# Kernel optimization log

Hardware: AMD Instinct MI355X
Metric: run time of the kernel (lower is better)

Reference implementation:

```python
import jax, jax.numpy as jnp
import numpy as np

BS, S = 8, 1024
D_MODEL, N_HEADS, D_K = 256, 8, 32
H_SHARED, H_SEL = 2, 2
N_DYN = N_HEADS - H_SHARED
D_FF = 1024
N_BLOCKS = 2
L = 3 * N_BLOCKS  # blocks_1 (N_BLOCKS layers) + blocks_2 (2*N_BLOCKS layers)
NEG = -1e9


def _layernorm(x, g, b):
    m = x.mean(-1, keepdims=True)
    v = ((x - m) ** 2).mean(-1, keepdims=True)
    return (x - m) * jax.lax.rsqrt(v + 1e-5) * g + b


def _layer(p, mask_val, query, values, q4router, apply_pos):
    (Wq, bq, Wv, bv, Wg, Wo, bo, g1, be1, Wf1, bf1, Wf2, bf2, g2, be2) = p
    bs, s, dm = query.shape
    q = query @ Wq + bq            # kq_same=True -> k = q
    v = values @ Wv + bv
    qh = q.reshape(bs, s, N_HEADS, D_K).transpose(0, 2, 1, 3)   # [b,h,s,d]
    vh = v.reshape(bs, s, N_HEADS, D_K).transpose(0, 2, 1, 3)
    scores = jnp.einsum('bhqd,bhkd->bhqk', qh, qh) / (D_K ** 0.5)
    # nopeek = triu(ones,k=mask); allowed where nopeek==0 -> col < row + mask
    allowed = jnp.arange(s)[None, :] < (jnp.arange(s)[:, None] + mask_val)
    scores = jnp.where(allowed[None, None], scores, NEG)
    attnw = jax.nn.softmax(scores, axis=-1)
    # head routing: replicate torch view->permute->reshape order exactly
    qr = q4router.reshape(bs, s, N_HEADS, D_K).transpose(0, 2, 1, 3).reshape(bs * s, N_HEADS * D_K)
    gates = jax.nn.softmax(qr @ Wg, axis=1)                     # [bs*s, N_DYN]
    _, idx = jax.lax.top_k(gates, H_SEL)
    dyn_mask = jax.nn.one_hot(idx, N_DYN, dtype=gates.dtype).sum(axis=1)
    dyn_scores = gates * dyn_mask
    hs = dyn_mask.sum(axis=0)
    hp = gates.mean(axis=0)
    bal = ((hs / (hs.sum() + 1e-5)) * (hp / (hp.sum() + 1e-5))).sum()
    routing = jnp.concatenate(
        [jnp.ones((bs, s, H_SHARED), gates.dtype), dyn_scores.reshape(bs, s, N_DYN)], axis=-1)
    routing = routing.mean(axis=1)[:, :, None, None]            # [b,h,1,1]
    out = jnp.einsum('bhqk,bhkd->bhqd', attnw, vh) * routing
    out = out.transpose(0, 2, 1, 3).reshape(bs, s, dm) @ Wo + bo
    query = _layernorm(query + out, g1, be1)
    if apply_pos:
        ff = jax.nn.relu(query @ Wf1 + bf1) @ Wf2 + bf2
        query = _layernorm(query + ff, g2, be2)
    return query, bal


def _forward(q_embed_data, qa_embed_data, Wq, bq, Wv, bv, Wg, Wo, bo,
             ln1_w, ln1_b, Wf1, bf1, Wf2, bf2, ln2_w, ln2_b):
    stacks = (Wq, bq, Wv, bv, Wg, Wo, bo, ln1_w, ln1_b, Wf1, bf1, Wf2, bf2, ln2_w, ln2_b)
    params = [tuple(a[i] for a in stacks) for i in range(L)]
    x, y = q_embed_data, qa_embed_data
    for i in range(N_BLOCKS):
        y, _ = _layer(params[i], 1, y, y, x, True)
    attn = jnp.zeros((), jnp.float32)
    li = N_BLOCKS
    for _ in range(N_BLOCKS):
        x, _ = _layer(params[li], 1, x, x, x, False)  # self-block, no FFN
        li += 1
        x, attn = _layer(params[li], 0, x, y, x, True)  # cross to y, strict causal
        li += 1
    return x, attn


def setup_inputs():
    key = jax.random.key(0)
    ks = jax.random.split(key, 10)
    w = lambda k, shp: (jax.random.normal(k, shp, jnp.float32) * 0.02)
    return {
        'q_embed_data': jax.random.normal(ks[0], (BS, S, D_MODEL), jnp.float32),
        'qa_embed_data': jax.random.normal(ks[1], (BS, S, D_MODEL), jnp.float32),
        'Wq': w(ks[2], (L, D_MODEL, D_MODEL)), 'bq': jnp.zeros((L, D_MODEL), jnp.float32),
        'Wv': w(ks[3], (L, D_MODEL, D_MODEL)), 'bv': jnp.zeros((L, D_MODEL), jnp.float32),
        'Wg': w(ks[4], (L, D_MODEL, N_DYN)),
        'Wo': w(ks[5], (L, D_MODEL, D_MODEL)), 'bo': jnp.zeros((L, D_MODEL), jnp.float32),
        'ln1_w': jnp.ones((L, D_MODEL), jnp.float32), 'ln1_b': jnp.zeros((L, D_MODEL), jnp.float32),
        'Wf1': w(ks[6], (L, D_MODEL, D_FF)), 'bf1': jnp.zeros((L, D_FF), jnp.float32),
        'Wf2': w(ks[7], (L, D_FF, D_MODEL)), 'bf2': jnp.zeros((L, D_MODEL), jnp.float32),
        'ln2_w': jnp.ones((L, D_MODEL), jnp.float32), 'ln2_b': jnp.zeros((L, D_MODEL), jnp.float32),
    }


def reference(q_embed_data, qa_embed_data, Wq, bq, Wv, bv, Wg, Wo, bo,
              ln1_w, ln1_b, Wf1, bf1, Wf2, bf2, ln2_w, ln2_b):
    return _forward(q_embed_data, qa_embed_data, Wq, bq, Wv, bv, Wg, Wo, bo,
                    ln1_w, ln1_b, Wf1, bf1, Wf2, bf2, ln2_w, ln2_b)
```

## Files before the change

kernel.cpp:

```cpp
#include <hip/hip_runtime.h>


constexpr int DMODEL = 256;
constexpr int SEQ    = 1024;
constexpr int BATCH  = 8;
constexpr int NHEADS = 8;
constexpr int DKDIM  = 32;
constexpr int NDYN_C = 6;
constexpr int NTOK_C = BATCH * SEQ;
constexpr int DFF_C  = 1024;

using frag_bf16 = __attribute__((ext_vector_type(8))) short;
using f32x4    = __attribute__((ext_vector_type(4))) float;
typedef unsigned short ushort_t;

__device__ __forceinline__ ushort_t f2bf(float f) {
  unsigned u = __float_as_uint(f);
  unsigned r = (u + 0x7fffu + ((u >> 16) & 1u)) >> 16;
  return (ushort_t)r;
}

__device__ __forceinline__ unsigned cvt_pk_bf16(float lo, float hi) {
  unsigned r;
  asm("v_cvt_pk_bf16_f32 %0, %1, %2" : "=v"(r) : "v"(lo), "v"(hi));
  return r;
}

#define GLOAD_LDS16(gsrc, ldst)                                             \
  __builtin_amdgcn_global_load_lds(                                         \
      (const __attribute__((address_space(1))) void*)(gsrc),                \
      (__attribute__((address_space(3))) void*)(ldst), 16, 0, 0)

#define SYNC_DRAIN()                                                        \
  do {                                                                      \
    asm volatile("s_waitcnt vmcnt(0) lgkmcnt(0)" ::: "memory");             \
    __builtin_amdgcn_sched_barrier(0);                                      \
    __syncthreads();                                                        \
  } while (0)

__device__ __forceinline__
void gemm_body(int mode, int bx, int by,
               const ushort_t* __restrict__ A, const ushort_t* __restrict__ B,
               const float* __restrict__ bias, void* __restrict__ Cp,
               int M, int N, int K,
               ushort_t (*sA)[4096], ushort_t (*sB)[4096]) {
  const int tid = threadIdx.x;
  const int wid = tid >> 6, lane = tid & 63;
  const int li = lane & 15, g = lane >> 4;
  const int wr = wid >> 1, wc = wid & 1;
  const int m0 = by * 64, n0 = bx * 64;
  f32x4 acc[2][2] = {};
  const int srow = wid * 8 + (lane >> 3);
  const int schk = (lane & 7) ^ (lane >> 3);
  const ushort_t* gA1 = &A[(size_t)(m0 + srow) * K + schk * 8];
  const ushort_t* gA2 = &A[(size_t)(m0 + 32 + srow) * K + schk * 8];
  const ushort_t* gB1 = &B[(size_t)(n0 + srow) * K + schk * 8];
  const ushort_t* gB2 = &B[(size_t)(n0 + 32 + srow) * K + schk * 8];
  const int nk = K >> 6;

  GLOAD_LDS16(gA1, sA[0] + wid * 512);
  GLOAD_LDS16(gA2, sA[0] + 2048 + wid * 512);
  GLOAD_LDS16(gB1, sB[0] + wid * 512);
  GLOAD_LDS16(gB2, sB[0] + 2048 + wid * 512);
  SYNC_DRAIN();

  auto compute = [&](int cur) {
#pragma unroll
    for (int s = 0; s < 2; ++s) {
      frag_bf16 af[2], bf[2];
#pragma unroll
      for (int m = 0; m < 2; ++m) {
        const int row = wr * 32 + m * 16 + li;
        af[m] = *reinterpret_cast<const frag_bf16*>(
            &sA[cur][row * 64 + ((s * 4 + g) ^ (row & 7)) * 8]);
      }
#pragma unroll
      for (int n = 0; n < 2; ++n) {
        const int row = wc * 32 + n * 16 + li;
        bf[n] = *reinterpret_cast<const frag_bf16*>(
            &sB[cur][row * 64 + ((s * 4 + g) ^ (row & 7)) * 8]);
      }
#pragma unroll
      for (int m = 0; m < 2; ++m)
#pragma unroll
        for (int n = 0; n < 2; ++n)
          acc[m][n] = __builtin_amdgcn_mfma_f32_16x16x32_bf16(af[m], bf[n], acc[m][n], 0, 0, 0);
    }
  };

  for (int kt = 0; kt < nk - 1; ++kt) {
    const int cur = kt & 1;
    const int k1 = (kt + 1) << 6;
    GLOAD_LDS16(gA1 + k1, sA[cur ^ 1] + wid * 512);
    GLOAD_LDS16(gA2 + k1, sA[cur ^ 1] + 2048 + wid * 512);
    GLOAD_LDS16(gB1 + k1, sB[cur ^ 1] + wid * 512);
    GLOAD_LDS16(gB2 + k1, sB[cur ^ 1] + 2048 + wid * 512);
    compute(cur);
    SYNC_DRAIN();
  }
  compute((nk - 1) & 1);

  constexpr float QSCALE = 0.42044820762685725f;
#pragma unroll
  for (int m = 0; m < 2; ++m)
#pragma unroll
    for (int n = 0; n < 2; ++n)
#pragma unroll
      for (int r = 0; r < 4; ++r) {
        const int mg = m0 + wr * 32 + m * 16 + g * 4 + r;
        const int ng = n0 + wc * 32 + n * 16 + li;
        if (mode == 0) {
          ((float*)Cp)[(size_t)mg * N + ng] = acc[m][n][r] + bias[ng];
        } else if (mode == 1) {
          ((ushort_t*)Cp)[(size_t)mg * N + ng] = f2bf((acc[m][n][r] + bias[ng]) * QSCALE);
        } else if (mode == 2) {
          ((ushort_t*)Cp)[(size_t)mg * N + ng] = f2bf(fmaxf(acc[m][n][r] + bias[ng], 0.0f));
        } else {
          ((ushort_t*)Cp)[((size_t)((ng >> 10) * 256 + mg)) * SEQ + (ng & 1023)] =
              f2bf(acc[m][n][r] + bias[mg]);
        }
      }
}

__global__ __launch_bounds__(256)
void gemm_mfma_k(int mode, const ushort_t* __restrict__ A, const ushort_t* __restrict__ B,
                 const float* __restrict__ bias, void* __restrict__ Cp,
                 int M, int N, int K) {
  __shared__ ushort_t sA[2][4096];
  __shared__ ushort_t sB[2][4096];
  gemm_body(mode, blockIdx.x, blockIdx.y, A, B, bias, Cp, M, N, K, sA, sB);
}

__device__ __forceinline__
void router_body(const float* __restrict__ R, const float* __restrict__ Wg,
                 float* __restrict__ partials, float* sW, float (*red)[128]) {
  const int tid = threadIdx.x;
  for (int t = tid; t < DMODEL * NDYN_C; t += 256) sW[t] = Wg[t];
  __syncthreads();
  if (tid < 128) {
    const int r = blockIdx.x * 128 + tid;
    const int b = r >> 10;
    const int h = (r >> 7) & 7;
    const int s8 = r & 127;
    float lg[NDYN_C] = {};
    for (int t8 = 0; t8 < 8; ++t8) {
      const float* base = &R[((size_t)(b * SEQ + s8 * 8 + t8)) * DMODEL + h * DKDIM];
#pragma unroll
      for (int d = 0; d < DKDIM; ++d) {
        const float x = base[d];
        const float* w = &sW[(t8 * 32 + d) * NDYN_C];
#pragma unroll
        for (int j = 0; j < NDYN_C; ++j) lg[j] = fmaf(x, w[j], lg[j]);
      }
    }
    float mx = lg[0];
#pragma unroll
    for (int j = 1; j < NDYN_C; ++j) mx = fmaxf(mx, lg[j]);
    float e[NDYN_C], sum = 0.0f;
#pragma unroll
    for (int j = 0; j < NDYN_C; ++j) { e[j] = expf(lg[j] - mx); sum += e[j]; }
    float g[NDYN_C];
#pragma unroll
    for (int j = 0; j < NDYN_C; ++j) g[j] = e[j] / sum;
    int j1 = 0;
#pragma unroll
    for (int j = 1; j < NDYN_C; ++j) if (g[j] > g[j1]) j1 = j;
    int j2 = -1;
#pragma unroll
    for (int j = 0; j < NDYN_C; ++j) {
      if (j == j1) continue;
      if (j2 < 0 || g[j] > g[j2]) j2 = j;
    }
#pragma unroll
    for (int j = 0; j < NDYN_C; ++j) {
      const bool sel = (j == j1) || (j == j2);
      red[j][tid] = sel ? g[j] : 0.0f;
      red[6 + j][tid] = sel ? 1.0f : 0.0f;
      red[12 + j][tid] = g[j];
    }
  }
  __syncthreads();
  if (tid < 18) {
    float s = 0.0f;
    for (int i = 0; i < 128; ++i) s += red[tid][i];
    partials[blockIdx.x * 18 + tid] = s;
  }
}

__global__ __launch_bounds__(256)
void gemm_qv_router_k(const ushort_t* __restrict__ Aq, const ushort_t* __restrict__ Bq,
                      const float* __restrict__ biasq, void* __restrict__ Cq,
                      const ushort_t* __restrict__ Av, const ushort_t* __restrict__ Bv,
                      const float* __restrict__ biasv, void* __restrict__ Cv,
                      const float* __restrict__ R, const float* __restrict__ Wg,
                      float* __restrict__ partials) {
  __shared__ ushort_t sA[2][4096];
  __shared__ ushort_t sB[2][4096];
  if (blockIdx.y == 4) {
    if (blockIdx.z == 0 && blockIdx.x < 64) {
      float* sW = (float*)&sA[0][0];
      float (*red)[128] = (float(*)[128])&sB[0][0];
      router_body(R, Wg, partials, sW, red);
    }
    return;
  }
  if (blockIdx.z == 0)
    gemm_body(1, blockIdx.y, blockIdx.x, Aq, Bq, biasq, Cq, NTOK_C, DMODEL, DMODEL, sA, sB);
  else
    gemm_body(3, blockIdx.x, blockIdx.y, Av, Bv, biasv, Cv, DMODEL, NTOK_C, DMODEL, sA, sB);
}

__device__ __forceinline__
void transpose_body(const float* __restrict__ ip, ushort_t* __restrict__ op, int R, int C,
                    int c0, int r0) {
  __shared__ float t[32][33];
  const int tx = threadIdx.x & 31, ty = threadIdx.x >> 5;
#pragma unroll
  for (int i = 0; i < 4; ++i) t[ty + 8 * i][tx] = ip[(size_t)(r0 + ty + 8 * i) * C + c0 + tx];
  __syncthreads();
#pragma unroll
  for (int i = 0; i < 4; ++i)
    op[(size_t)(c0 + ty + 8 * i) * R + r0 + tx] = f2bf(t[tx][ty + 8 * i]);
}

__global__ __launch_bounds__(256)
void transpose_k(const float* __restrict__ in, ushort_t* __restrict__ out, int R, int C) {
  const int z = blockIdx.z;
  transpose_body(in + (size_t)z * R * C, out + (size_t)z * R * C, R, C,
                 blockIdx.x * 32, blockIdx.y * 32);
}

__global__ __launch_bounds__(256)
void transpose3_k(const float* __restrict__ W0, ushort_t* __restrict__ O0,
                  const float* __restrict__ W1, ushort_t* __restrict__ O1,
                  const float* __restrict__ W2, ushort_t* __restrict__ O2) {
  const int z = blockIdx.z;
  const int zi = z / 6, zz = z % 6;
  const float* in = (zi == 0) ? W0 : (zi == 1) ? W1 : W2;
  ushort_t* out = (zi == 0) ? O0 : (zi == 1) ? O1 : O2;
  transpose_body(in + (size_t)zz * DMODEL * DMODEL, out + (size_t)zz * DMODEL * DMODEL,
                 DMODEL, DMODEL, blockIdx.x * 32, blockIdx.y * 32);
}

__global__ __launch_bounds__(256)
void conv_init_k(const float* __restrict__ s0, float* __restrict__ f0,
                 ushort_t* __restrict__ b0,
                 const float* __restrict__ s1, float* __restrict__ f1,
                 ushort_t* __restrict__ b1) {
  const float* src = blockIdx.y ? s1 : s0;
  float* dstF = blockIdx.y ? f1 : f0;
  ushort_t* dstB = blockIdx.y ? b1 : b0;
  const int i = blockIdx.x * 256 + threadIdx.x;
  const float4 v = reinterpret_cast<const float4*>(src)[i];
  reinterpret_cast<float4*>(dstF)[i] = v;
  ushort4 b;
  b.x = f2bf(v.x); b.y = f2bf(v.y); b.z = f2bf(v.z); b.w = f2bf(v.w);
  reinterpret_cast<ushort4*>(dstB)[i] = b;
}

__global__ __launch_bounds__(256)
void attn_mfma_k(const ushort_t* __restrict__ qb, const ushort_t* __restrict__ vbT,
                 const float* __restrict__ partials, ushort_t* __restrict__ out,
                 int mask_val) {
  __shared__ ushort_t sk[2][2048];
  __shared__ ushort_t sv[2][2048];
  __shared__ ushort_t pbuf[4096];
  const int gid = blockIdx.x;
  const int b = gid & 7;
  const int slot = gid >> 3;
  const int h = (slot >> 4) & 7;
  const int qblk = 15 - (slot & 15);
  const int q0 = qblk * 64;
  const int tid = threadIdx.x;
  const int wave = tid >> 6, lane = tid & 63;
  const int g = lane >> 4, li = lane & 15;
  const int qw = q0 + wave * 16;
  const int qrow = qw + li;

  const frag_bf16 qf = *reinterpret_cast<const frag_bf16*>(
      &qb[((size_t)(b * SEQ + qrow)) * DMODEL + h * DKDIM + g * 8]);

  float mrun = -INFINITY, lrun = 0.f;
  f32x4 o0 = {0.f, 0.f, 0.f, 0.f}, o1 = {0.f, 0.f, 0.f, 0.f};
  ushort_t* pP = &pbuf[wave * 1024];

  const ushort_t* gK = &qb[((size_t)(b * SEQ + wave * 16 + li)) * DMODEL + h * DKDIM + g * 8];
  const ushort_t* gV = &vbT[((size_t)((b * NHEADS + h) * DKDIM) + wave * 8 + (lane >> 3)) * SEQ
                            + ((lane & 7) ^ (lane >> 3)) * 8];

  const int nt = qblk + 1;
  GLOAD_LDS16(gK, sk[0] + wave * 512);
  GLOAD_LDS16(gV, sv[0] + wave * 512);
  SYNC_DRAIN();

  auto tile_step = [&](int t, int cur) {
    const int kt = t * 64;
    f32x4 s[4];
#pragma unroll
    for (int kb = 0; kb < 4; ++kb) {
      frag_bf16 kf = *reinterpret_cast<const frag_bf16*>(&sk[cur][(kb * 64 + g * 16 + li) * 8]);
      f32x4 z = {0.f, 0.f, 0.f, 0.f};
      s[kb] = __builtin_amdgcn_mfma_f32_16x16x32_bf16(kf, qf, z, 0, 0, 0);
    }
    const bool need_mask = (kt + 63) >= (qw + mask_val);
    if (need_mask) {
#pragma unroll
      for (int kb = 0; kb < 4; ++kb)
#pragma unroll
        for (int r = 0; r < 4; ++r) {
          const int col = kt + kb * 16 + 4 * g + r;
          if (col >= (qrow + mask_val)) s[kb][r] = -1e9f;
        }
    }
    float tm = -INFINITY;
#pragma unroll
    for (int kb = 0; kb < 4; ++kb)
#pragma unroll
      for (int r = 0; r < 4; ++r) tm = fmaxf(tm, s[kb][r]);
    tm = fmaxf(tm, __shfl_xor(tm, 16, 64));
    tm = fmaxf(tm, __shfl_xor(tm, 32, 64));
    const float mnew = fmaxf(mrun, tm);
    const float scl = __expf(mrun - mnew);
    float p[4][4];
    float psum = 0.f;
#pragma unroll
    for (int kb = 0; kb < 4; ++kb)
#pragma unroll
      for (int r = 0; r < 4; ++r) { p[kb][r] = __expf(s[kb][r] - mnew); psum += p[kb][r]; }
    psum += __shfl_xor(psum, 16, 64);
    psum += __shfl_xor(psum, 32, 64);
    lrun = lrun * scl + psum;
    mrun = mnew;
#pragma unroll
    for (int r = 0; r < 4; ++r) { o0[r] *= scl; o1[r] *= scl; }
#pragma unroll
    for (int kb = 0; kb < 4; ++kb)
#pragma unroll
      for (int pair = 0; pair < 2; ++pair) {
        const unsigned pk = cvt_pk_bf16(p[kb][2 * pair], p[kb][2 * pair + 1]);
        const int addr = (((kb >> 1) * 4 + (kb & 1) * 2 + (g >> 1)) * 16 + li) * 8
                         + 4 * (g & 1) + 2 * pair;
        *reinterpret_cast<unsigned*>(&pP[addr]) = pk;
      }
    __threadfence_block();
#pragma unroll
    for (int c = 0; c < 2; ++c) {
      frag_bf16 pf = *reinterpret_cast<const frag_bf16*>(&pP[((c * 4 + g) * 16 + li) * 8]);
      frag_bf16 vf0 = *reinterpret_cast<const frag_bf16*>(
          &sv[cur][li * 64 + ((4 * c + g) ^ (li & 7)) * 8]);
      frag_bf16 vf1 = *reinterpret_cast<const frag_bf16*>(
          &sv[cur][(16 + li) * 64 + ((4 * c + g) ^ (li & 7)) * 8]);
      o0 = __builtin_amdgcn_mfma_f32_16x16x32_bf16(vf0, pf, o0, 0, 0, 0);
      o1 = __builtin_amdgcn_mfma_f32_16x16x32_bf16(vf1, pf, o1, 0, 0, 0);
    }
  };

  for (int t = 0; t < nt - 1; ++t) {
    const int cur = t & 1;
    const int kt = t * 64;
    GLOAD_LDS16(gK + (size_t)(kt + 64) * DMODEL, sk[cur ^ 1] + wave * 512);
    GLOAD_LDS16(gV + (kt + 64), sv[cur ^ 1] + wave * 512);
    tile_step(t, cur);
    SYNC_DRAIN();
  }
  tile_step(nt - 1, (nt - 1) & 1);

  float rt = 1.0f;
  if (h >= 2) {
    const int j = h - 2;
    float sr = 0.f;
#pragma unroll
    for (int t = 0; t < 8; ++t) sr += partials[(b * 8 + t) * 18 + j];
    rt = sr * (1.0f / 1024.0f);
  }
  const float mult = rt / lrun;
  if (!(mask_val == 0 && qrow == 0)) {
    const size_t base = (size_t)(b * SEQ + qrow) * DMODEL + h * DKDIM;
    ushort4 w0, w1;
    w0.x = f2bf(o0[0] * mult); w0.y = f2bf(o0[1] * mult);
    w0.z = f2bf(o0[2] * mult); w0.w = f2bf(o0[3] * mult);
    w1.x = f2bf(o1[0] * mult); w1.y = f2bf(o1[1] * mult);
    w1.z = f2bf(o1[2] * mult); w1.w = f2bf(o1[3] * mult);
    *reinterpret_cast<ushort4*>(&out[base + 4 * g]) = w0;
    *reinterpret_cast<ushort4*>(&out[base + 16 + 4 * g]) = w1;
  }
  if (mask_val == 0 && qblk == 0 && wave == 0) {
    const int d = lane >> 1, hf = lane & 1;
    const ushort_t* src = &vbT[(((size_t)(b * NHEADS + h)) * DKDIM + d) * SEQ + hf * 512];
    float s = 0.f;
    for (int k = 0; k < 512; k += 8) {
      frag_bf16 v = *reinterpret_cast<const frag_bf16*>(&src[k]);
#pragma unroll
      for (int j = 0; j < 8; ++j)
        s += __uint_as_float(((unsigned)(ushort_t)v[j]) << 16);
    }
    s += __shfl_xor(s, 1, 64);
    if (hf == 0)
      out[(size_t)(b * SEQ) * DMODEL + h * DKDIM + d] = f2bf(s * (1.0f / 1024.0f) * rt);
  }
}

__global__ void router_reduce_k(const float* __restrict__ partials,
                                float* __restrict__ bal_out) {
  const int tid = threadIdx.x;
  if (tid == 0) {
    float hs[6], hp[6];
    float hssum = 0.0f, hpsum = 0.0f;
    for (int j = 0; j < 6; ++j) {
      float a = 0.0f, c = 0.0f;
      for (int bi = 0; bi < 64; ++bi) {
        a += partials[bi * 18 + 6 + j];
        c += partials[bi * 18 + 12 + j];
      }
      hs[j] = a;
      hp[j] = c * (1.0f / 8192.0f);
      hssum += hs[j];
      hpsum += hp[j];
    }
    float bal = 0.0f;
    for (int j = 0; j < 6; ++j)
      bal += (hs[j] / (hssum + 1e-5f)) * (hp[j] / (hpsum + 1e-5f));
    *bal_out = bal;
  }
}

__global__ __launch_bounds__(256)
void add_ln_k(const float* __restrict__ Xin, float* __restrict__ Xout,
              ushort_t* __restrict__ Xbf, const float* __restrict__ Y,
              const float* __restrict__ g, const float* __restrict__ be) {
  const int wave = threadIdx.x >> 6, lane = threadIdx.x & 63;
  const int r = blockIdx.x * 4 + wave;
  const size_t base = (size_t)r * DMODEL + lane * 4;
  float4 x = *reinterpret_cast<const float4*>(&Xin[base]);
  const float4 y = *reinterpret_cast<const float4*>(&Y[base]);
  x.x += y.x; x.y += y.y; x.z += y.z; x.w += y.w;
  float s = x.x + x.y + x.z + x.w;
#pragma unroll
  for (int o = 32; o >= 1; o >>= 1) s += __shfl_xor(s, o, 64);
  const float mean = s * (1.0f / DMODEL);
  const float4 d = {x.x - mean, x.y - mean, x.z - mean, x.w - mean};
  float v = d.x * d.x + d.y * d.y + d.z * d.z + d.w * d.w;
#pragma unroll
  for (int o = 32; o >= 1; o >>= 1) v += __shfl_xor(v, o, 64);
  const float rstd = 1.0f / sqrtf(v * (1.0f / DMODEL) + 1e-5f);
  const float4 gg = *reinterpret_cast<const float4*>(&g[lane * 4]);
  const float4 bb = *reinterpret_cast<const float4*>(&be[lane * 4]);
  float4 rv;
  rv.x = d.x * rstd * gg.x + bb.x;
  rv.y = d.y * rstd * gg.y + bb.y;
  rv.z = d.z * rstd * gg.z + bb.z;
  rv.w = d.w * rstd * gg.w + bb.w;
  *reinterpret_cast<float4*>(&Xout[base]) = rv;
  ushort4 o4;
  o4.x = f2bf(rv.x); o4.y = f2bf(rv.y); o4.z = f2bf(rv.z); o4.w = f2bf(rv.w);
  *reinterpret_cast<ushort4*>(&Xbf[base]) = o4;
}

extern "C" void kernel_launch(void* const* d_in, const int* in_sizes, int n_in,
                              void* d_out, int out_size, void* d_ws, size_t ws_size,
                              hipStream_t stream) {
  const float* q_embed  = (const float*)d_in[0];
  const float* qa_embed = (const float*)d_in[1];
  const float* Wq  = (const float*)d_in[2];
  const float* bq  = (const float*)d_in[3];
  const float* Wv  = (const float*)d_in[4];
  const float* bv  = (const float*)d_in[5];
  const float* Wg  = (const float*)d_in[6];
  const float* Wo  = (const float*)d_in[7];
  const float* bo  = (const float*)d_in[8];
  const float* ln1w = (const float*)d_in[9];
  const float* ln1b = (const float*)d_in[10];
  const float* Wf1 = (const float*)d_in[11];
  const float* bf1 = (const float*)d_in[12];
  const float* Wf2 = (const float*)d_in[13];
  const float* bf2 = (const float*)d_in[14];
  const float* ln2w = (const float*)d_in[15];
  const float* ln2b = (const float*)d_in[16];
  float* out = (float*)d_out;

  const size_t NA = (size_t)NTOK_C * DMODEL;
  float* xbuf = (float*)d_ws;
  float* ybuf = xbuf + NA;
  float* ob   = ybuf + NA;
  float* routing8   = ob + NA;
  float* partials   = routing8 + 64;
  float* balscratch = partials + 64 * 18;
  ushort_t* xbf   = (ushort_t*)(balscratch + 16);
  ushort_t* ybf   = xbf + NA;
  ushort_t* qb_bf = ybf + NA;
  ushort_t* vbT   = qb_bf + NA;
  ushort_t* ab_bf = vbT + NA;
  ushort_t* hb    = ab_bf + NA;
  ushort_t* WqT   = hb + (size_t)NTOK_C * DFF_C;
  ushort_t* WvT   = WqT + (size_t)6 * DMODEL * DMODEL;
  ushort_t* WoT   = WvT + (size_t)6 * DMODEL * DMODEL;
  ushort_t* Wf1T  = WoT + (size_t)6 * DMODEL * DMODEL;
  ushort_t* Wf2T  = Wf1T + (size_t)6 * DMODEL * DFF_C;

  transpose3_k<<<dim3(8, 8, 18), 256, 0, stream>>>(Wq, WqT, Wv, WvT, Wo, WoT);
  transpose_k<<<dim3(32, 8, 6), 256, 0, stream>>>(Wf1, Wf1T, DMODEL, DFF_C);
  transpose_k<<<dim3(8, 32, 6), 256, 0, stream>>>(Wf2, Wf2T, DFF_C, DMODEL);
  conv_init_k<<<dim3(NA / 1024, 2), 256, 0, stream>>>(q_embed, xbuf, xbf,
                                                      qa_embed, ybuf, ybf);

  auto run_layer = [&](int l, float* Q, ushort_t* Qbf, const ushort_t* Vbf,
                       int mask_val, bool ffn, bool last) {
    const float* bq_l = bq + (size_t)l * DMODEL;
    const float* bv_l = bv + (size_t)l * DMODEL;
    const float* Wg_l = Wg + (size_t)l * DMODEL * NDYN_C;
    const float* bo_l = bo + (size_t)l * DMODEL;
    const float* g1_l = ln1w + (size_t)l * DMODEL;
    const float* b1_l = ln1b + (size_t)l * DMODEL;
    const ushort_t* WqT_l = WqT + (size_t)l * DMODEL * DMODEL;
    const ushort_t* WvT_l = WvT + (size_t)l * DMODEL * DMODEL;
    const ushort_t* WoT_l = WoT + (size_t)l * DMODEL * DMODEL;

    gemm_qv_router_k<<<dim3(128, 5, 2), 256, 0, stream>>>(
        Qbf, WqT_l, bq_l, qb_bf, WvT_l, Vbf, bv_l, vbT, xbuf, Wg_l, partials);
    if (last)
      router_reduce_k<<<1, 64, 0, stream>>>(partials, out + NA);
    attn_mfma_k<<<1024, 256, 0, stream>>>(qb_bf, vbT, partials, ab_bf, mask_val);
    gemm_mfma_k<<<dim3(4, 128), 256, 0, stream>>>(
        0, ab_bf, WoT_l, bo_l, ob, NTOK_C, DMODEL, DMODEL);
    add_ln_k<<<NTOK_C / 4, 256, 0, stream>>>(Q, Q, Qbf, ob, g1_l, b1_l);
    if (ffn) {
      const float* bf1_l = bf1 + (size_t)l * DFF_C;
      const float* bf2_l = bf2 + (size_t)l * DMODEL;
      const float* g2_l = ln2w + (size_t)l * DMODEL;
      const float* b2_l = ln2b + (size_t)l * DMODEL;
      const ushort_t* Wf1T_l = Wf1T + (size_t)l * DMODEL * DFF_C;
      const ushort_t* Wf2T_l = Wf2T + (size_t)l * DFF_C * DMODEL;
      gemm_mfma_k<<<dim3(16, 128), 256, 0, stream>>>(
          2, Qbf, Wf1T_l, bf1_l, hb, NTOK_C, DFF_C, DMODEL);
      gemm_mfma_k<<<dim3(4, 128), 256, 0, stream>>>(
          0, hb, Wf2T_l, bf2_l, ob, NTOK_C, DMODEL, DFF_C);
      add_ln_k<<<NTOK_C / 4, 256, 0, stream>>>(Q, last ? out : Q, Qbf, ob, g2_l, b2_l);
    }
  };

  run_layer(0, ybuf, ybf, ybf, 1, true, false);
  run_layer(1, ybuf, ybf, ybf, 1, true, false);
  run_layer(2, xbuf, xbf, xbf, 1, false, false);
  run_layer(3, xbuf, xbf, ybf, 0, true, false);
  run_layer(4, xbuf, xbf, xbf, 1, false, false);
  run_layer(5, xbuf, xbf, ybf, 0, true, true);
}
```

Measured before the change: 547.1 us.

## Fuse output/FFN2 GEMMs with residual add and LayerNorm epilogue

Adds a GEMM kernel where each block computes a full 32-row by 256-column output tile, so the residual add and LayerNorm can run in the epilogue using cross-wave shared-memory reductions. It replaces the separate Wo and Wf2 GEMMs plus add_ln kernels, which removes the float intermediate round-trip through global memory and one launch per use. In exchange the grid drops to 256 blocks with a large B tile in LDS, which lowers parallelism and occupancy. Variance is now computed as E[x^2]-mean^2, which is less numerically stable.

```diff
diff --git a/kernel.cpp b/kernel.cpp
--- a/kernel.cpp
+++ b/kernel.cpp
@@ -131,6 +131,125 @@
   gemm_body(mode, blockIdx.x, blockIdx.y, A, B, bias, Cp, M, N, K, sA, sB);
 }
 
+__global__ __launch_bounds__(256)
+void gemm_ln_k(const ushort_t* __restrict__ A, const ushort_t* __restrict__ B,
+               const float* __restrict__ bias,
+               const float* __restrict__ Xin, float* __restrict__ Xout,
+               ushort_t* __restrict__ Xbf,
+               const float* __restrict__ gam, const float* __restrict__ bet,
+               int K) {
+  __shared__ ushort_t sA[2][2048];
+  __shared__ ushort_t sB[2][16384];
+  __shared__ float ws1[4][32];
+  __shared__ float ws2[4][32];
+  const int tid = threadIdx.x;
+  const int wid = tid >> 6, lane = tid & 63;
+  const int li = lane & 15, g = lane >> 4;
+  const int wc = wid;
+  const int m0 = blockIdx.x * 32;
+  f32x4 acc[2][4] = {};
+  const int srow = tid >> 3;
+  const int schk = (tid & 7) ^ (srow & 7);
+  const ushort_t* gA = &A[(size_t)(m0 + srow) * K + schk * 8];
+  const ushort_t* gB = &B[(size_t)srow * K + schk * 8];
+  const int nk = K >> 6;
+
+  GLOAD_LDS16(gA, sA[0] + wid * 512);
+#pragma unroll
+  for (int i = 0; i < 8; ++i)
+    GLOAD_LDS16(gB + (size_t)i * 32 * K, sB[0] + i * 2048 + wid * 512);
+  SYNC_DRAIN();
+
+  auto compute = [&](int cur) {
+#pragma unroll
+    for (int s = 0; s < 2; ++s) {
+      frag_bf16 af[2], bf[4];
+#pragma unroll
+      for (int m = 0; m < 2; ++m) {
+        const int row = m * 16 + li;
+        af[m] = *reinterpret_cast<const frag_bf16*>(
+            &sA[cur][row * 64 + ((s * 4 + g) ^ (row & 7)) * 8]);
+      }
+#pragma unroll
+      for (int n = 0; n < 4; ++n) {
+        const int row = wc * 64 + n * 16 + li;
+        bf[n] = *reinterpret_cast<const frag_bf16*>(
+            &sB[cur][row * 64 + ((s * 4 + g) ^ (row & 7)) * 8]);
+      }
+#pragma unroll
+      for (int m = 0; m < 2; ++m)
+#pragma unroll
+        for (int n = 0; n < 4; ++n)
+          acc[m][n] = __builtin_amdgcn_mfma_f32_16x16x32_bf16(af[m], bf[n], acc[m][n], 0, 0, 0);
+    }
+  };
+
+  for (int kt = 0; kt < nk - 1; ++kt) {
+    const int cur = kt & 1;
+    const int k1 = (kt + 1) << 6;
+    GLOAD_LDS16(gA + k1, sA[cur ^ 1] + wid * 512);
+#pragma unroll
+    for (int i = 0; i < 8; ++i)
+      GLOAD_LDS16(gB + (size_t)i * 32 * K + k1, sB[cur ^ 1] + i * 2048 + wid * 512);
+    compute(cur);
+    SYNC_DRAIN();
+  }
+  compute((nk - 1) & 1);
+
+  float xv[2][4][4];
+  float s1[2][4] = {}, s2[2][4] = {};
+#pragma unroll
+  for (int m = 0; m < 2; ++m)
+#pragma unroll
+    for (int n = 0; n < 4; ++n)
+#pragma unroll
+      for (int r = 0; r < 4; ++r) {
+        const int row = m * 16 + g * 4 + r;
+        const int ng = wc * 64 + n * 16 + li;
+        const float x = acc[m][n][r] + bias[ng] + Xin[(size_t)(m0 + row) * DMODEL + ng];
+        xv[m][n][r] = x;
+        s1[m][r] += x;
+        s2[m][r] += x * x;
+      }
+#pragma unroll
+  for (int mask = 1; mask <= 8; mask <<= 1)
+#pragma unroll
+    for (int m = 0; m < 2; ++m)
+#pragma unroll
+      for (int r = 0; r < 4; ++r) {
+        s1[m][r] += __shfl_xor(s1[m][r], mask, 64);
+        s2[m][r] += __shfl_xor(s2[m][r], mask, 64);
+      }
+  if (li == 0) {
+#pragma unroll
+    for (int m = 0; m < 2; ++m)
+#pragma unroll
+      for (int r = 0; r < 4; ++r) {
+        ws1[wid][m * 16 + g * 4 + r] = s1[m][r];
+        ws2[wid][m * 16 + g * 4 + r] = s2[m][r];
+      }
+  }
+  __syncthreads();
+#pragma unroll
+  for (int m = 0; m < 2; ++m)
+#pragma unroll
+    for (int r = 0; r < 4; ++r) {
+      const int row = m * 16 + g * 4 + r;
+      const float S1 = ws1[0][row] + ws1[1][row] + ws1[2][row] + ws1[3][row];
+      const float S2 = ws2[0][row] + ws2[1][row] + ws2[2][row] + ws2[3][row];
+      const float mean = S1 * (1.0f / DMODEL);
+      const float var = fmaxf(S2 * (1.0f / DMODEL) - mean * mean, 0.0f);
+      const float rstd = 1.0f / sqrtf(var + 1e-5f);
+#pragma unroll
+      for (int n = 0; n < 4; ++n) {
+        const int ng = wc * 64 + n * 16 + li;
+        const float rv = (xv[m][n][r] - mean) * rstd * gam[ng] + bet[ng];
+        Xout[(size_t)(m0 + row) * DMODEL + ng] = rv;
+        Xbf[(size_t)(m0 + row) * DMODEL + ng] = f2bf(rv);
+      }
+    }
+}
+
 __device__ __forceinline__
 void router_body(const float* __restrict__ R, const float* __restrict__ Wg,
                  float* __restrict__ partials, float* sW, float (*red)[128]) {
@@ -402,8 +521,7 @@
 
 __global__ void router_reduce_k(const float* __restrict__ partials,
                                 float* __restrict__ bal_out) {
-  const int tid = threadIdx.x;
-  if (tid == 0) {
+  if (threadIdx.x == 0) {
     float hs[6], hp[6];
     float hssum = 0.0f, hpsum = 0.0f;
     for (int j = 0; j < 6; ++j) {
@@ -422,38 +540,6 @@
       bal += (hs[j] / (hssum + 1e-5f)) * (hp[j] / (hpsum + 1e-5f));
     *bal_out = bal;
   }
-}
-
-__global__ __launch_bounds__(256)
-void add_ln_k(const float* __restrict__ Xin, float* __restrict__ Xout,
-              ushort_t* __restrict__ Xbf, const float* __restrict__ Y,
-              const float* __restrict__ g, const float* __restrict__ be) {
-  const int wave = threadIdx.x >> 6, lane = threadIdx.x & 63;
-  const int r = blockIdx.x * 4 + wave;
-  const size_t base = (size_t)r * DMODEL + lane * 4;
-  float4 x = *reinterpret_cast<const float4*>(&Xin[base]);
-  const float4 y = *reinterpret_cast<const float4*>(&Y[base]);
-  x.x += y.x; x.y += y.y; x.z += y.z; x.w += y.w;
-  float s = x.x + x.y + x.z + x.w;
-#pragma unroll
-  for (int o = 32; o >= 1; o >>= 1) s += __shfl_xor(s, o, 64);
-  const float mean = s * (1.0f / DMODEL);
-  const float4 d = {x.x - mean, x.y - mean, x.z - mean, x.w - mean};
-  float v = d.x * d.x + d.y * d.y + d.z * d.z + d.w * d.w;
-#pragma unroll
-  for (int o = 32; o >= 1; o >>= 1) v += __shfl_xor(v, o, 64);
-  const float rstd = 1.0f / sqrtf(v * (1.0f / DMODEL) + 1e-5f);
-  const float4 gg = *reinterpret_cast<const float4*>(&g[lane * 4]);
-  const float4 bb = *reinterpret_cast<const float4*>(&be[lane * 4]);
-  float4 rv;
-  rv.x = d.x * rstd * gg.x + bb.x;
-  rv.y = d.y * rstd * gg.y + bb.y;
-  rv.z = d.z * rstd * gg.z + bb.z;
-  rv.w = d.w * rstd * gg.w + bb.w;
-  *reinterpret_cast<float4*>(&Xout[base]) = rv;
-  ushort4 o4;
-  o4.x = f2bf(rv.x); o4.y = f2bf(rv.y); o4.z = f2bf(rv.z); o4.w = f2bf(rv.w);
-  *reinterpret_cast<ushort4*>(&Xbf[base]) = o4;
 }
 
 extern "C" void kernel_launch(void* const* d_in, const int* in_sizes, int n_in,
@@ -520,9 +606,8 @@
     if (last)
       router_reduce_k<<<1, 64, 0, stream>>>(partials, out + NA);
     attn_mfma_k<<<1024, 256, 0, stream>>>(qb_bf, vbT, partials, ab_bf, mask_val);
-    gemm_mfma_k<<<dim3(4, 128), 256, 0, stream>>>(
-        0, ab_bf, WoT_l, bo_l, ob, NTOK_C, DMODEL, DMODEL);
-    add_ln_k<<<NTOK_C / 4, 256, 0, stream>>>(Q, Q, Qbf, ob, g1_l, b1_l);
+    gemm_ln_k<<<256, 256, 0, stream>>>(ab_bf, WoT_l, bo_l, Q, Q, Qbf,
+                                       g1_l, b1_l, DMODEL);
     if (ffn) {
       const float* bf1_l = bf1 + (size_t)l * DFF_C;
       const float* bf2_l = bf2 + (size_t)l * DMODEL;
@@ -532,9 +617,8 @@
       const ushort_t* Wf2T_l = Wf2T + (size_t)l * DFF_C * DMODEL;
       gemm_mfma_k<<<dim3(16, 128), 256, 0, stream>>>(
           2, Qbf, Wf1T_l, bf1_l, hb, NTOK_C, DFF_C, DMODEL);
-      gemm_mfma_k<<<dim3(4, 128), 256, 0, stream>>>(
-          0, hb, Wf2T_l, bf2_l, ob, NTOK_C, DMODEL, DFF_C);
-      add_ln_k<<<NTOK_C / 4, 256, 0, stream>>>(Q, last ? out : Q, Qbf, ob, g2_l, b2_l);
+      gemm_ln_k<<<256, 256, 0, stream>>>(hb, Wf2T_l, bf2_l, Q, last ? out : Q, Qbf,
+                                         g2_l, b2_l, DFF_C);
     }
   };
 
```

Result: no change. 547.6 us (+0.1%).
